# Optimization experiments

Hardware: AMD Instinct MI355X
Metric: run time of the kernel (lower is better)

The kernel has to match this reference:

```python
import jax, jax.numpy as jnp
import numpy as np

GH, GW = 16, 16          # group_size
DIM = 512
H = 8                    # num_heads
PD = DIM // 16           # pos_dim = (dim//4)//4 = 32
B = 256                  # number of groups (batch*windows)
N = GH * GW


def _make_bias_tables():
    # biases buffer: all 2D relative offsets, shape [(2GH-1)*(2GW-1), 2]
    h = np.arange(1 - GH, GH)
    w = np.arange(1 - GW, GW)
    bh, bw = np.meshgrid(h, w, indexing='ij')
    biases = np.stack([bh, bw]).reshape(2, -1).T.astype(np.float32)
    # relative_position_index: [N, N] lookup into the bias table
    ch, cw = np.meshgrid(np.arange(GH), np.arange(GW), indexing='ij')
    coords = np.stack([ch, cw]).reshape(2, -1)            # [2, N]
    rel = coords[:, :, None] - coords[:, None, :]         # [2, N, N]
    rel = rel.transpose(1, 2, 0).copy()                   # [N, N, 2]
    rel[:, :, 0] += GH - 1
    rel[:, :, 1] += GW - 1
    rel[:, :, 0] *= 2 * GW - 1
    idx = rel.sum(-1)
    return biases, idx.astype(np.int32)


def _ln(x, g, b, eps=1e-5):
    m = x.mean(-1, keepdims=True)
    v = ((x - m) ** 2).mean(-1, keepdims=True)
    return (x - m) / jnp.sqrt(v + eps) * g + b


def setup_inputs() -> dict:
    key = jax.random.key(0)
    ks = jax.random.split(key, 16)
    s = 0.02
    biases_np, idx_np = _make_bias_tables()
    return {
        'x': jax.random.normal(ks[0], (B, N, DIM), dtype=jnp.float32),
        'qkv_w': jax.random.normal(ks[1], (DIM, 3 * DIM), dtype=jnp.float32) * s,
        'qkv_b': jnp.zeros((3 * DIM,), jnp.float32),
        'proj_w': jax.random.normal(ks[2], (DIM, DIM), dtype=jnp.float32) * s,
        'proj_b': jnp.zeros((DIM,), jnp.float32),
        'p1_w': jax.random.normal(ks[3], (2, PD), dtype=jnp.float32) * s,
        'p1_b': jnp.zeros((PD,), jnp.float32),
        'g1': jnp.ones((PD,), jnp.float32), 'b1': jnp.zeros((PD,), jnp.float32),
        'p2_w': jax.random.normal(ks[4], (PD, PD), dtype=jnp.float32) * s,
        'p2_b': jnp.zeros((PD,), jnp.float32),
        'g2': jnp.ones((PD,), jnp.float32), 'b2': jnp.zeros((PD,), jnp.float32),
        'p3_w': jax.random.normal(ks[5], (PD, PD), dtype=jnp.float32) * s,
        'p3_b': jnp.zeros((PD,), jnp.float32),
        'g3': jnp.ones((PD,), jnp.float32), 'b3': jnp.zeros((PD,), jnp.float32),
        'p4_w': jax.random.normal(ks[6], (PD, H), dtype=jnp.float32) * s,
        'p4_b': jnp.zeros((H,), jnp.float32),
        'biases': jnp.asarray(biases_np),
        'rel_idx': jnp.asarray(idx_np),
    }


def reference(x, qkv_w, qkv_b, proj_w, proj_b,
              p1_w, p1_b, g1, b1, p2_w, p2_b, g2, b2,
              p3_w, p3_b, g3, b3, p4_w, p4_b, biases, rel_idx):
    Bn, Nn, C = x.shape
    hd = C // H
    scale = hd ** -0.5
    qkv = (x @ qkv_w + qkv_b).reshape(Bn, Nn, 3, H, hd).transpose(2, 0, 3, 1, 4)
    q, k, v = qkv[0] * scale, qkv[1], qkv[2]      # [B, H, N, hd]
    attn = jnp.einsum('bhnd,bhmd->bhnm', q, k)    # [B, H, N, N]
    # dynamic position bias MLP on the offset table
    h1 = jax.nn.relu(_ln(biases @ p1_w + p1_b, g1, b1))
    h2 = jax.nn.relu(_ln(h1 @ p2_w + p2_b, g2, b2))
    h3 = jax.nn.relu(_ln(h2 @ p3_w + p3_b, g3, b3))
    pos = h3 @ p4_w + p4_b                        # [L, H]
    rpb = pos[rel_idx.reshape(-1)].reshape(Nn, Nn, H).transpose(2, 0, 1)  # [H, N, N]
    attn = jax.nn.softmax(attn + rpb[None], axis=-1)
    out = jnp.einsum('bhnm,bhmd->bhnd', attn, v)
    out = out.transpose(0, 2, 1, 3).reshape(Bn, Nn, C)
    return out @ proj_w + proj_b
```

## Files before the change

kernel.cpp:

```cpp
#include <hip/hip_runtime.h>
#include <stdint.h>

typedef __bf16 bf16x8 __attribute__((ext_vector_type(8)));
typedef float  f32x4  __attribute__((ext_vector_type(4)));
typedef unsigned short ushort_t;

#define MFMA16(a,b,c) __builtin_amdgcn_mfma_f32_16x16x32_bf16((a),(b),(c),0,0,0)

#define GLOAD16(gsrc, ldst) \
    __builtin_amdgcn_global_load_lds((const __attribute__((address_space(1))) void*)(gsrc), \
                                     (__attribute__((address_space(3))) void*)(ldst), 16, 0, 0)

#define BATCH 256
#define NTOK  256
#define DIM   512
#define NH    8
#define HD    64
#define PD    32
#define LTAB  961

#define POS_OFF   0
#define RPB_OFF   32768
#define WQKV_OFF  (RPB_OFF + 2097152)
#define WPROJ_OFF (WQKV_OFF + 1572864)
#define QKV_OFF   (WPROJ_OFF + 524288)
#define AOUT_OFF  (QKV_OFF + 201326592)
#define XB_OFF    AOUT_OFF

__device__ __forceinline__ ushort_t f2bf(float f) {
    unsigned int u = __builtin_bit_cast(unsigned int, f);
    u += 0x7FFFu + ((u >> 16) & 1u);
    return (ushort_t)(u >> 16);
}

__global__ __launch_bounds__(256) void convert_x(
    const float* __restrict__ x, ushort_t* __restrict__ xb)
{
    size_t i = ((size_t)blockIdx.x * 256 + threadIdx.x) * 8;
    float4 f0 = *(const float4*)(x + i);
    float4 f1 = *(const float4*)(x + i + 4);
    uint4 o;
    o.x = (unsigned)f2bf(f0.x) | ((unsigned)f2bf(f0.y) << 16);
    o.y = (unsigned)f2bf(f0.z) | ((unsigned)f2bf(f0.w) << 16);
    o.z = (unsigned)f2bf(f1.x) | ((unsigned)f2bf(f1.y) << 16);
    o.w = (unsigned)f2bf(f1.z) | ((unsigned)f2bf(f1.w) << 16);
    *reinterpret_cast<uint4*>(xb + i) = o;
}

__global__ __launch_bounds__(256) void transpose_w(
    const float* __restrict__ src, ushort_t* __restrict__ dst, int K, int Nn)
{
    __shared__ ushort_t tile[64][65];
    int tiles_n = Nn >> 6;
    int tn = blockIdx.x % tiles_n, tk = blockIdx.x / tiles_n;
    int n0 = tn * 64, k0 = tk * 64;
    int t = threadIdx.x;
#pragma unroll
    for (int i = 0; i < 16; i++) {
        int idx = t + i * 256;
        int kl = idx >> 6, nl = idx & 63;
        tile[nl][kl] = f2bf(src[(size_t)(k0 + kl) * Nn + n0 + nl]);
    }
    __syncthreads();
#pragma unroll
    for (int i = 0; i < 16; i++) {
        int idx = t + i * 256;
        int nl = idx >> 6, kl = idx & 63;
        dst[(size_t)(n0 + nl) * K + k0 + kl] = tile[nl][kl];
    }
}

__device__ __forceinline__ float ln_relu_t(float h, int j,
                                           const float* __restrict__ g,
                                           const float* __restrict__ bb) {
    float m = h;
    m += __shfl_xor(m, 1); m += __shfl_xor(m, 2); m += __shfl_xor(m, 4);
    m += __shfl_xor(m, 8); m += __shfl_xor(m, 16);
    m *= (1.0f / PD);
    float d = h - m;
    float v = d * d;
    v += __shfl_xor(v, 1); v += __shfl_xor(v, 2); v += __shfl_xor(v, 4);
    v += __shfl_xor(v, 8); v += __shfl_xor(v, 16);
    v *= (1.0f / PD);
    float x = d * rsqrtf(v + 1e-5f) * g[j] + bb[j];
    return x > 0.f ? x : 0.f;
}

__global__ __launch_bounds__(256) void pos_mlp(
    const float* __restrict__ biases,
    const float* __restrict__ p1_w, const float* __restrict__ p1_b,
    const float* __restrict__ g1, const float* __restrict__ b1,
    const float* __restrict__ p2_w, const float* __restrict__ p2_b,
    const float* __restrict__ g2, const float* __restrict__ b2,
    const float* __restrict__ p3_w, const float* __restrict__ p3_b,
    const float* __restrict__ g3, const float* __restrict__ b3,
    const float* __restrict__ p4_w, const float* __restrict__ p4_b,
    float* __restrict__ pos)
{
    __shared__ float hs[8][33];
    int tid = threadIdx.x;
    int rl = tid >> 5, j = tid & 31;
    int r = blockIdx.x * 8 + rl;
    bool ok = r < LTAB;
    float c0 = ok ? biases[r * 2 + 0] : 0.f;
    float c1 = ok ? biases[r * 2 + 1] : 0.f;

    float h = c0 * p1_w[j] + c1 * p1_w[PD + j] + p1_b[j];
    h = ln_relu_t(h, j, g1, b1);

    hs[rl][j] = h;
    __syncthreads();
    float s = p2_b[j];
#pragma unroll
    for (int i = 0; i < PD; i++) s += hs[rl][i] * p2_w[i * PD + j];
    __syncthreads();
    h = ln_relu_t(s, j, g2, b2);

    hs[rl][j] = h;
    __syncthreads();
    s = p3_b[j];
#pragma unroll
    for (int i = 0; i < PD; i++) s += hs[rl][i] * p3_w[i * PD + j];
    __syncthreads();
    h = ln_relu_t(s, j, g3, b3);

    hs[rl][j] = h;
    __syncthreads();
    if (ok && j < NH) {
        float o = p4_b[j];
#pragma unroll
        for (int i = 0; i < PD; i++) o += hs[rl][i] * p4_w[i * NH + j];
        pos[r * NH + j] = o;
    }
}

__global__ __launch_bounds__(256) void rpb_gather(
    const float* __restrict__ pos, const int* __restrict__ rel_idx,
    float* __restrict__ rpb)
{
    int i = blockIdx.x * 256 + threadIdx.x;
    int idx = rel_idx[i];
#pragma unroll
    for (int hh = 0; hh < NH; hh++) rpb[(size_t)hh * 65536 + i] = pos[idx * NH + hh];
}

__global__ __launch_bounds__(512, 1) void qkv_gemm(
    const ushort_t* __restrict__ xb, const ushort_t* __restrict__ wT,
    const float* __restrict__ qkv_b, ushort_t* __restrict__ qkvb)
{
    __shared__ ushort_t As[2][256 * 64];
    __shared__ ushort_t Bs[2][256 * 64];
    int t = threadIdx.x;
    int bid = blockIdx.x;
    int wgid = (bid & 7) * 192 + (bid >> 3);
    int mt = wgid / 6, nt = wgid % 6;
    int m0 = mt * 256, n0 = nt * 256;
    int lane = t & 63, w = t >> 6;
    int wm = w >> 2, wn = w & 3;
    int lr = lane & 15, lk = lane >> 4;
    int srow8 = lane >> 3;
    int sch = ((lane & 7) ^ srow8) * 8;
    const ushort_t* Asrc = xb + (size_t)(m0 + srow8) * 512 + sch;
    const ushort_t* Bsrc = wT + (size_t)(n0 + srow8) * 512 + sch;
    int arw = w & 3;
    int ch0 = ((lk) ^ (lr & 7)) * 8;
    int ch1 = ((4 + lk) ^ (lr & 7)) * 8;
    int arow = wm * 128 + lr;
    int brow = wn * 64 + lr;

    f32x4 acc[8][4];
#pragma unroll
    for (int fr = 0; fr < 8; fr++)
#pragma unroll
        for (int fc = 0; fc < 4; fc++) acc[fr][fc] = (f32x4){0.f, 0.f, 0.f, 0.f};

#define QSTAGE(buf, kt) do { \
    if (w < 4) { \
        _Pragma("unroll") \
        for (int i_ = 0; i_ < 8; i_++) { \
            int rb_ = arw * 64 + i_ * 8; \
            GLOAD16(Asrc + (size_t)rb_ * 512 + (kt) * 64, &As[buf][rb_ * 64]); \
        } \
    } else { \
        _Pragma("unroll") \
        for (int i_ = 0; i_ < 8; i_++) { \
            int rb_ = arw * 64 + i_ * 8; \
            GLOAD16(Bsrc + (size_t)rb_ * 512 + (kt) * 64, &Bs[buf][rb_ * 64]); \
        } \
    } } while (0)

    QSTAGE(0, 0);
    asm volatile("s_waitcnt vmcnt(0)" ::: "memory");
    __syncthreads();
    for (int kt = 0; kt < 8; ++kt) {
        int cb = kt & 1;
        if (kt < 7) QSTAGE(cb ^ 1, kt + 1);
#pragma unroll
        for (int kh = 0; kh < 2; kh++) {
            int ch = kh ? ch1 : ch0;
            bf16x8 a[8], b[4];
#pragma unroll
            for (int fr = 0; fr < 8; fr++)
                a[fr] = *reinterpret_cast<const bf16x8*>(&As[cb][(arow + fr * 16) * 64 + ch]);
#pragma unroll
            for (int fc = 0; fc < 4; fc++)
                b[fc] = *reinterpret_cast<const bf16x8*>(&Bs[cb][(brow + fc * 16) * 64 + ch]);
#pragma unroll
            for (int fr = 0; fr < 8; fr++)
#pragma unroll
                for (int fc = 0; fc < 4; fc++)
                    acc[fr][fc] = MFMA16(a[fr], b[fc], acc[fr][fc]);
        }
        if (kt < 7) {
            asm volatile("s_waitcnt vmcnt(0)" ::: "memory");
            __syncthreads();
        }
    }
#undef QSTAGE

    int s = n0 >> 9;
    int bg = m0 >> 8;
    if (s < 2) {
        float sc = (s == 0) ? 0.125f : 1.0f;
#pragma unroll
        for (int fc = 0; fc < 4; fc++) {
            int n = n0 + wn * 64 + fc * 16 + lr;
            float bias = qkv_b[n];
            int hh = (n >> 6) & 7, d = n & 63;
            ushort_t* dst = qkvb + ((((size_t)s * 256 + bg) * 8 + hh) * 256) * 64 + d;
#pragma unroll
            for (int fr = 0; fr < 8; fr++)
#pragma unroll
                for (int r = 0; r < 4; r++) {
                    int tok = wm * 128 + fr * 16 + lk * 4 + r;
                    dst[(size_t)tok * 64] = f2bf((acc[fr][fc][r] + bias) * sc);
                }
        }
    } else {
#pragma unroll
        for (int fc = 0; fc < 4; fc++) {
            int n = n0 + wn * 64 + fc * 16 + lr;
            float bias = qkv_b[n];
            int hh = (n >> 6) & 7, d = n & 63;
            ushort_t* dst = qkvb + ((((size_t)512 + bg) * 8 + hh) * 64 + d) * 256;
#pragma unroll
            for (int fr = 0; fr < 8; fr++) {
                int tok = wm * 128 + fr * 16 + lk * 4;
                uint2 pk;
                pk.x = (unsigned)f2bf(acc[fr][fc][0] + bias) |
                       ((unsigned)f2bf(acc[fr][fc][1] + bias) << 16);
                pk.y = (unsigned)f2bf(acc[fr][fc][2] + bias) |
                       ((unsigned)f2bf(acc[fr][fc][3] + bias) << 16);
                *reinterpret_cast<uint2*>(dst + tok) = pk;
            }
        }
    }
}

__global__ __launch_bounds__(256) void attn_kernel(
    const ushort_t* __restrict__ qkvb, const float* __restrict__ rpb,
    ushort_t* __restrict__ aout)
{
    __shared__ ushort_t Ps[4][32][40];
    __shared__ ushort_t Os[4][16 * 72];
    int t = threadIdx.x, lane = t & 63, w = t >> 6;
    int bid = blockIdx.x;
    int qh = bid & 1; int bh = bid >> 1; int hh = bh & 7; int bg = bh >> 3;
    const ushort_t* Qg  = qkvb + (((size_t)bg * 8 + hh) * 256) * 64;
    const ushort_t* Kg  = qkvb + (((size_t)(256 + bg) * 8 + hh) * 256) * 64;
    const ushort_t* VTg = qkvb + (((size_t)(512 + bg) * 8 + hh) * 64) * 256;
    int lr = lane & 15, lk = lane >> 4;
    int qrow0 = qh * 128 + w * 32;

    bf16x8 qf[2][2];
#pragma unroll
    for (int fr = 0; fr < 2; fr++)
#pragma unroll
        for (int kc = 0; kc < 2; kc++)
            qf[fr][kc] = *reinterpret_cast<const bf16x8*>(
                Qg + (size_t)(qrow0 + fr * 16 + lr) * 64 + kc * 32 + lk * 8);

    f32x4 oacc[2][4];
    float rsum[2][4];
#pragma unroll
    for (int fr = 0; fr < 2; fr++) {
#pragma unroll
        for (int fc = 0; fc < 4; fc++) oacc[fr][fc] = (f32x4){0.f, 0.f, 0.f, 0.f};
#pragma unroll
        for (int r = 0; r < 4; r++) rsum[fr][r] = 0.f;
    }

    for (int kt = 0; kt < 8; ++kt) {
        f32x4 sacc[2][2];
#pragma unroll
        for (int fr = 0; fr < 2; fr++)
#pragma unroll
            for (int fc = 0; fc < 2; fc++) sacc[fr][fc] = (f32x4){0.f, 0.f, 0.f, 0.f};
#pragma unroll
        for (int kc = 0; kc < 2; kc++) {
            bf16x8 kb0 = *reinterpret_cast<const bf16x8*>(
                Kg + (size_t)(kt * 32 + lr) * 64 + kc * 32 + lk * 8);
            bf16x8 kb1 = *reinterpret_cast<const bf16x8*>(
                Kg + (size_t)(kt * 32 + 16 + lr) * 64 + kc * 32 + lk * 8);
            sacc[0][0] = MFMA16(qf[0][kc], kb0, sacc[0][0]);
            sacc[0][1] = MFMA16(qf[0][kc], kb1, sacc[0][1]);
            sacc[1][0] = MFMA16(qf[1][kc], kb0, sacc[1][0]);
            sacc[1][1] = MFMA16(qf[1][kc], kb1, sacc[1][1]);
        }
#pragma unroll
        for (int fr = 0; fr < 2; fr++)
#pragma unroll
            for (int fc = 0; fc < 2; fc++)
#pragma unroll
                for (int r = 0; r < 4; r++) {
                    int row = qrow0 + fr * 16 + lk * 4 + r;
                    int col = kt * 32 + fc * 16 + lr;
                    float lg = sacc[fr][fc][r] + rpb[((size_t)hh * 256 + row) * 256 + col];
                    float p = __expf(lg);
                    rsum[fr][r] += p;
                    Ps[w][fr * 16 + lk * 4 + r][fc * 16 + lr] = f2bf(p);
                }
        bf16x8 pa[2], vb[4];
#pragma unroll
        for (int fr = 0; fr < 2; fr++)
            pa[fr] = *reinterpret_cast<const bf16x8*>(&Ps[w][fr * 16 + lr][lk * 8]);
#pragma unroll
        for (int fc = 0; fc < 4; fc++)
            vb[fc] = *reinterpret_cast<const bf16x8*>(
                VTg + (size_t)(fc * 16 + lr) * 256 + kt * 32 + lk * 8);
#pragma unroll
        for (int fr = 0; fr < 2; fr++)
#pragma unroll
            for (int fc = 0; fc < 4; fc++)
                oacc[fr][fc] = MFMA16(pa[fr], vb[fc], oacc[fr][fc]);
    }
    float rinv[2][4];
#pragma unroll
    for (int fr = 0; fr < 2; fr++)
#pragma unroll
        for (int r = 0; r < 4; r++) {
            float s = rsum[fr][r];
            s += __shfl_xor(s, 1); s += __shfl_xor(s, 2);
            s += __shfl_xor(s, 4); s += __shfl_xor(s, 8);
            rinv[fr][r] = __frcp_rn(s);
        }
#pragma unroll
    for (int fr = 0; fr < 2; fr++) {
#pragma unroll
        for (int fc = 0; fc < 4; fc++)
#pragma unroll
            for (int r = 0; r < 4; r++)
                Os[w][(lk * 4 + r) * 72 + fc * 16 + lr] = f2bf(oacc[fr][fc][r] * rinv[fr][r]);
#pragma unroll
        for (int ii = 0; ii < 2; ii++) {
            int j = lane + ii * 64;
            int row = j >> 3, ch = j & 7;
            uint4 v = *reinterpret_cast<const uint4*>(&Os[w][row * 72 + ch * 8]);
            *reinterpret_cast<uint4*>(
                aout + ((size_t)(bg * 256 + qrow0 + fr * 16 + row)) * 512 + hh * 64 + ch * 8) = v;
        }
    }
}

__global__ __launch_bounds__(512, 1) void proj_gemm(
    const ushort_t* __restrict__ ain, const ushort_t* __restrict__ wT,
    const float* __restrict__ proj_b, float* __restrict__ out)
{
    __shared__ ushort_t As[2][256 * 64];
    __shared__ ushort_t Bs[2][256 * 64];
    int t = threadIdx.x;
    int bid = blockIdx.x;
    int wgid = (bid & 7) * 64 + (bid >> 3);
    int mt = wgid / 2, nt = wgid % 2;
    int m0 = mt * 256, n0 = nt * 256;
    int lane = t & 63, w = t >> 6;
    int wm = w >> 2, wn = w & 3;
    int lr = lane & 15, lk = lane >> 4;
    int srow8 = lane >> 3;
    int sch = ((lane & 7) ^ srow8) * 8;
    const ushort_t* Asrc = ain + (size_t)(m0 + srow8) * 512 + sch;
    const ushort_t* Bsrc = wT + (size_t)(n0 + srow8) * 512 + sch;
    int arw = w & 3;
    int ch0 = ((lk) ^ (lr & 7)) * 8;
    int ch1 = ((4 + lk) ^ (lr & 7)) * 8;
    int arow = wm * 128 + lr;
    int brow = wn * 64 + lr;

    f32x4 acc[8][4];
#pragma unroll
    for (int fr = 0; fr < 8; fr++)
#pragma unroll
        for (int fc = 0; fc < 4; fc++) acc[fr][fc] = (f32x4){0.f, 0.f, 0.f, 0.f};

#define PSTAGE(buf, kt) do { \
    if (w < 4) { \
        _Pragma("unroll") \
        for (int i_ = 0; i_ < 8; i_++) { \
            int rb_ = arw * 64 + i_ * 8; \
            GLOAD16(Asrc + (size_t)rb_ * 512 + (kt) * 64, &As[buf][rb_ * 64]); \
        } \
    } else { \
        _Pragma("unroll") \
        for (int i_ = 0; i_ < 8; i_++) { \
            int rb_ = arw * 64 + i_ * 8; \
            GLOAD16(Bsrc + (size_t)rb_ * 512 + (kt) * 64, &Bs[buf][rb_ * 64]); \
        } \
    } } while (0)

    PSTAGE(0, 0);
    asm volatile("s_waitcnt vmcnt(0)" ::: "memory");
    __syncthreads();
    for (int kt = 0; kt < 8; ++kt) {
        int cb = kt & 1;
        if (kt < 7) PSTAGE(cb ^ 1, kt + 1);
#pragma unroll
        for (int kh = 0; kh < 2; kh++) {
            int ch = kh ? ch1 : ch0;
            bf16x8 a[8], b[4];
#pragma unroll
            for (int fr = 0; fr < 8; fr++)
                a[fr] = *reinterpret_cast<const bf16x8*>(&As[cb][(arow + fr * 16) * 64 + ch]);
#pragma unroll
            for (int fc = 0; fc < 4; fc++)
                b[fc] = *reinterpret_cast<const bf16x8*>(&Bs[cb][(brow + fc * 16) * 64 + ch]);
#pragma unroll
            for (int fr = 0; fr < 8; fr++)
#pragma unroll
                for (int fc = 0; fc < 4; fc++)
                    acc[fr][fc] = MFMA16(a[fr], b[fc], acc[fr][fc]);
        }
        if (kt < 7) {
            asm volatile("s_waitcnt vmcnt(0)" ::: "memory");
            __syncthreads();
        }
    }
#undef PSTAGE
#pragma unroll
    for (int fc = 0; fc < 4; fc++) {
        int n = n0 + wn * 64 + fc * 16 + lr;
        float bias = proj_b[n];
#pragma unroll
        for (int fr = 0; fr < 8; fr++)
#pragma unroll
            for (int r = 0; r < 4; r++) {
                int m = m0 + wm * 128 + fr * 16 + lk * 4 + r;
                out[(size_t)m * 512 + n] = acc[fr][fc][r] + bias;
            }
    }
}

extern "C" void kernel_launch(void* const* d_in, const int* in_sizes, int n_in,
                              void* d_out, int out_size, void* d_ws, size_t ws_size,
                              hipStream_t stream) {
    const float* x      = (const float*)d_in[0];
    const float* qkv_w  = (const float*)d_in[1];
    const float* qkv_b  = (const float*)d_in[2];
    const float* proj_w = (const float*)d_in[3];
    const float* proj_b = (const float*)d_in[4];
    const float* p1_w = (const float*)d_in[5];
    const float* p1_b = (const float*)d_in[6];
    const float* g1   = (const float*)d_in[7];
    const float* b1   = (const float*)d_in[8];
    const float* p2_w = (const float*)d_in[9];
    const float* p2_b = (const float*)d_in[10];
    const float* g2   = (const float*)d_in[11];
    const float* b2   = (const float*)d_in[12];
    const float* p3_w = (const float*)d_in[13];
    const float* p3_b = (const float*)d_in[14];
    const float* g3   = (const float*)d_in[15];
    const float* b3   = (const float*)d_in[16];
    const float* p4_w = (const float*)d_in[17];
    const float* p4_b = (const float*)d_in[18];
    const float* biases  = (const float*)d_in[19];
    const int*   rel_idx = (const int*)d_in[20];
    float* out = (float*)d_out;

    char* ws = (char*)d_ws;
    float*    pos    = (float*)(ws + POS_OFF);
    float*    rpb    = (float*)(ws + RPB_OFF);
    ushort_t* wqkvT  = (ushort_t*)(ws + WQKV_OFF);
    ushort_t* wprojT = (ushort_t*)(ws + WPROJ_OFF);
    ushort_t* qkvb   = (ushort_t*)(ws + QKV_OFF);
    ushort_t* aoutb  = (ushort_t*)(ws + AOUT_OFF);
    ushort_t* xb     = (ushort_t*)(ws + XB_OFF);

    convert_x<<<dim3(16384), dim3(256), 0, stream>>>(x, xb);
    transpose_w<<<dim3(24 * 8), dim3(256), 0, stream>>>(qkv_w, wqkvT, 512, 1536);
    transpose_w<<<dim3(8 * 8), dim3(256), 0, stream>>>(proj_w, wprojT, 512, 512);
    pos_mlp<<<dim3(121), dim3(256), 0, stream>>>(biases, p1_w, p1_b, g1, b1,
                                                 p2_w, p2_b, g2, b2,
                                                 p3_w, p3_b, g3, b3,
                                                 p4_w, p4_b, pos);
    rpb_gather<<<dim3(256), dim3(256), 0, stream>>>(pos, rel_idx, rpb);
    qkv_gemm<<<dim3(1536), dim3(512), 0, stream>>>(xb, wqkvT, qkv_b, qkvb);
    attn_kernel<<<dim3(4096), dim3(256), 0, stream>>>(qkvb, rpb, aoutb);
    proj_gemm<<<dim3(512), dim3(512), 0, stream>>>(aoutb, wprojT, proj_b, out);
}
```

Before: 383.0 us.

## Deepen qkv/proj GEMM pipeline with half-K LDS stages and MFMA priority

The qkv and proj GEMMs now split each 64-wide K tile into two 32-wide half stages. All waves issue loads for both A and B, and loads run up to three half-stages ahead, with partial vmcnt waits in place of the full drain. The LDS swizzle changes to fit 32-element rows, and s_setprio raises wave priority around the MFMA blocks. The goal is to hide global-to-LDS latency behind compute, at the cost of more barriers and tighter waitcnt bookkeeping, where a miscount could cause races.

```diff
diff --git a/kernel.cpp b/kernel.cpp
--- a/kernel.cpp
+++ b/kernel.cpp
@@ -148,8 +148,8 @@
     const ushort_t* __restrict__ xb, const ushort_t* __restrict__ wT,
     const float* __restrict__ qkv_b, ushort_t* __restrict__ qkvb)
 {
-    __shared__ ushort_t As[2][256 * 64];
-    __shared__ ushort_t Bs[2][256 * 64];
+    __shared__ ushort_t As[2][2][8192];
+    __shared__ ushort_t Bs[2][2][8192];
     int t = threadIdx.x;
     int bid = blockIdx.x;
     int wgid = (bid & 7) * 192 + (bid >> 3);
@@ -158,13 +158,11 @@
     int lane = t & 63, w = t >> 6;
     int wm = w >> 2, wn = w & 3;
     int lr = lane & 15, lk = lane >> 4;
-    int srow8 = lane >> 3;
-    int sch = ((lane & 7) ^ srow8) * 8;
-    const ushort_t* Asrc = xb + (size_t)(m0 + srow8) * 512 + sch;
-    const ushort_t* Bsrc = wT + (size_t)(n0 + srow8) * 512 + sch;
-    int arw = w & 3;
-    int ch0 = ((lk) ^ (lr & 7)) * 8;
-    int ch1 = ((4 + lk) ^ (lr & 7)) * 8;
+    int srow = lane >> 2;
+    int sch = ((lane & 3) ^ ((lane >> 3) & 3)) * 8;
+    const ushort_t* Asrc = xb + (size_t)(m0 + srow) * 512 + sch;
+    const ushort_t* Bsrc = wT + (size_t)(n0 + srow) * 512 + sch;
+    int rch = (lk ^ ((lr >> 1) & 3)) * 8;
     int arow = wm * 128 + lr;
     int brow = wn * 64 + lr;
 
@@ -174,49 +172,53 @@
 #pragma unroll
         for (int fc = 0; fc < 4; fc++) acc[fr][fc] = (f32x4){0.f, 0.f, 0.f, 0.f};
 
-#define QSTAGE(buf, kt) do { \
-    if (w < 4) { \
+#define QSTAGE(buf, kt, kh) do { \
+    _Pragma("unroll") \
+    for (int j_ = 0; j_ < 2; j_++) { \
+        int r0_ = (w * 2 + j_) * 16; \
+        GLOAD16(Asrc + (size_t)r0_ * 512 + (kt) * 64 + (kh) * 32, &As[buf][kh][r0_ * 32]); \
+        GLOAD16(Bsrc + (size_t)r0_ * 512 + (kt) * 64 + (kh) * 32, &Bs[buf][kh][r0_ * 32]); \
+    } } while (0)
+
+#define QCOMP(cb, kh) do { \
+    bf16x8 a_[8], b_[4]; \
+    _Pragma("unroll") \
+    for (int fr = 0; fr < 8; fr++) \
+        a_[fr] = *reinterpret_cast<const bf16x8*>(&As[cb][kh][(arow + fr * 16) * 32 + rch]); \
+    _Pragma("unroll") \
+    for (int fc = 0; fc < 4; fc++) \
+        b_[fc] = *reinterpret_cast<const bf16x8*>(&Bs[cb][kh][(brow + fc * 16) * 32 + rch]); \
+    __builtin_amdgcn_s_setprio(1); \
+    _Pragma("unroll") \
+    for (int fr = 0; fr < 8; fr++) \
         _Pragma("unroll") \
-        for (int i_ = 0; i_ < 8; i_++) { \
-            int rb_ = arw * 64 + i_ * 8; \
-            GLOAD16(Asrc + (size_t)rb_ * 512 + (kt) * 64, &As[buf][rb_ * 64]); \
-        } \
-    } else { \
-        _Pragma("unroll") \
-        for (int i_ = 0; i_ < 8; i_++) { \
-            int rb_ = arw * 64 + i_ * 8; \
-            GLOAD16(Bsrc + (size_t)rb_ * 512 + (kt) * 64, &Bs[buf][rb_ * 64]); \
-        } \
-    } } while (0)
-
-    QSTAGE(0, 0);
-    asm volatile("s_waitcnt vmcnt(0)" ::: "memory");
+        for (int fc = 0; fc < 4; fc++) \
+            acc[fr][fc] = MFMA16(a_[fr], b_[fc], acc[fr][fc]); \
+    __builtin_amdgcn_s_setprio(0); \
+    } while (0)
+
+    QSTAGE(0, 0, 0);
+    QSTAGE(0, 0, 1);
+    QSTAGE(1, 1, 0);
+    asm volatile("s_waitcnt vmcnt(8)" ::: "memory");
     __syncthreads();
     for (int kt = 0; kt < 8; ++kt) {
         int cb = kt & 1;
-        if (kt < 7) QSTAGE(cb ^ 1, kt + 1);
-#pragma unroll
-        for (int kh = 0; kh < 2; kh++) {
-            int ch = kh ? ch1 : ch0;
-            bf16x8 a[8], b[4];
-#pragma unroll
-            for (int fr = 0; fr < 8; fr++)
-                a[fr] = *reinterpret_cast<const bf16x8*>(&As[cb][(arow + fr * 16) * 64 + ch]);
-#pragma unroll
-            for (int fc = 0; fc < 4; fc++)
-                b[fc] = *reinterpret_cast<const bf16x8*>(&Bs[cb][(brow + fc * 16) * 64 + ch]);
-#pragma unroll
-            for (int fr = 0; fr < 8; fr++)
-#pragma unroll
-                for (int fc = 0; fc < 4; fc++)
-                    acc[fr][fc] = MFMA16(a[fr], b[fc], acc[fr][fc]);
-        }
+        if (kt + 1 < 8) QSTAGE((kt + 1) & 1, kt + 1, 1);
+        QCOMP(cb, 0);
+        if (kt < 7) asm volatile("s_waitcnt vmcnt(8)" ::: "memory");
+        else        asm volatile("s_waitcnt vmcnt(0)" ::: "memory");
+        __syncthreads();
+        if (kt + 2 < 8) QSTAGE(cb, kt + 2, 0);
+        QCOMP(cb, 1);
         if (kt < 7) {
-            asm volatile("s_waitcnt vmcnt(0)" ::: "memory");
+            if (kt == 6) asm volatile("s_waitcnt vmcnt(4)" ::: "memory");
+            else         asm volatile("s_waitcnt vmcnt(8)" ::: "memory");
             __syncthreads();
         }
     }
 #undef QSTAGE
+#undef QCOMP
 
     int s = n0 >> 9;
     int bg = m0 >> 8;
@@ -366,8 +368,8 @@
     const ushort_t* __restrict__ ain, const ushort_t* __restrict__ wT,
     const float* __restrict__ proj_b, float* __restrict__ out)
 {
-    __shared__ ushort_t As[2][256 * 64];
-    __shared__ ushort_t Bs[2][256 * 64];
+    __shared__ ushort_t As[2][2][8192];
+    __shared__ ushort_t Bs[2][2][8192];
     int t = threadIdx.x;
     int bid = blockIdx.x;
     int wgid = (bid & 7) * 64 + (bid >> 3);
@@ -376,13 +378,11 @@
     int lane = t & 63, w = t >> 6;
     int wm = w >> 2, wn = w & 3;
     int lr = lane & 15, lk = lane >> 4;
-    int srow8 = lane >> 3;
-    int sch = ((lane & 7) ^ srow8) * 8;
-    const ushort_t* Asrc = ain + (size_t)(m0 + srow8) * 512 + sch;
-    const ushort_t* Bsrc = wT + (size_t)(n0 + srow8) * 512 + sch;
-    int arw = w & 3;
-    int ch0 = ((lk) ^ (lr & 7)) * 8;
-    int ch1 = ((4 + lk) ^ (lr & 7)) * 8;
+    int srow = lane >> 2;
+    int sch = ((lane & 3) ^ ((lane >> 3) & 3)) * 8;
+    const ushort_t* Asrc = ain + (size_t)(m0 + srow) * 512 + sch;
+    const ushort_t* Bsrc = wT + (size_t)(n0 + srow) * 512 + sch;
+    int rch = (lk ^ ((lr >> 1) & 3)) * 8;
     int arow = wm * 128 + lr;
     int brow = wn * 64 + lr;
 
@@ -392,49 +392,54 @@
 #pragma unroll
         for (int fc = 0; fc < 4; fc++) acc[fr][fc] = (f32x4){0.f, 0.f, 0.f, 0.f};
 
-#define PSTAGE(buf, kt) do { \
-    if (w < 4) { \
+#define PSTAGE(buf, kt, kh) do { \
+    _Pragma("unroll") \
+    for (int j_ = 0; j_ < 2; j_++) { \
+        int r0_ = (w * 2 + j_) * 16; \
+        GLOAD16(Asrc + (size_t)r0_ * 512 + (kt) * 64 + (kh) * 32, &As[buf][kh][r0_ * 32]); \
+        GLOAD16(Bsrc + (size_t)r0_ * 512 + (kt) * 64 + (kh) * 32, &Bs[buf][kh][r0_ * 32]); \
+    } } while (0)
+
+#define PCOMP(cb, kh) do { \
+    bf16x8 a_[8], b_[4]; \
+    _Pragma("unroll") \
+    for (int fr = 0; fr < 8; fr++) \
+        a_[fr] = *reinterpret_cast<const bf16x8*>(&As[cb][kh][(arow + fr * 16) * 32 + rch]); \
+    _Pragma("unroll") \
+    for (int fc = 0; fc < 4; fc++) \
+        b_[fc] = *reinterpret_cast<const bf16x8*>(&Bs[cb][kh][(brow + fc * 16) * 32 + rch]); \
+    __builtin_amdgcn_s_setprio(1); \
+    _Pragma("unroll") \
+    for (int fr = 0; fr < 8; fr++) \
         _Pragma("unroll") \
-        for (int i_ = 0; i_ < 8; i_++) { \
-            int rb_ = arw * 64 + i_ * 8; \
-            GLOAD16(Asrc + (size_t)rb_ * 512 + (kt) * 64, &As[buf][rb_ * 64]); \
-        } \
-    } else { \
-        _Pragma("unroll") \
-        for (int i_ = 0; i_ < 8; i_++) { \
-            int rb_ = arw * 64 + i_ * 8; \
-            GLOAD16(Bsrc + (size_t)rb_ * 512 + (kt) * 64, &Bs[buf][rb_ * 64]); \
-        } \
-    } } while (0)
-
-    PSTAGE(0, 0);
-    asm volatile("s_waitcnt vmcnt(0)" ::: "memory");
+        for (int fc = 0; fc < 4; fc++) \
+            acc[fr][fc] = MFMA16(a_[fr], b_[fc], acc[fr][fc]); \
+    __builtin_amdgcn_s_setprio(0); \
+    } while (0)
+
+    PSTAGE(0, 0, 0);
+    PSTAGE(0, 0, 1);
+    PSTAGE(1, 1, 0);
+    asm volatile("s_waitcnt vmcnt(8)" ::: "memory");
     __syncthreads();
     for (int kt = 0; kt < 8; ++kt) {
         int cb = kt & 1;
-        if (kt < 7) PSTAGE(cb ^ 1, kt + 1);
-#pragma unroll
-        for (int kh = 0; kh < 2; kh++) {
-            int ch = kh ? ch1 : ch0;
-            bf16x8 a[8], b[4];
-#pragma unroll
-            for (int fr = 0; fr < 8; fr++)
-                a[fr] = *reinterpret_cast<const bf16x8*>(&As[cb][(arow + fr * 16) * 64 + ch]);
-#pragma unroll
-            for (int fc = 0; fc < 4; fc++)
-                b[fc] = *reinterpret_cast<const bf16x8*>(&Bs[cb][(brow + fc * 16) * 64 + ch]);
-#pragma unroll
-            for (int fr = 0; fr < 8; fr++)
-#pragma unroll
-                for (int fc = 0; fc < 4; fc++)
-                    acc[fr][fc] = MFMA16(a[fr], b[fc], acc[fr][fc]);
-        }
+        if (kt + 1 < 8) PSTAGE((kt + 1) & 1, kt + 1, 1);
+        PCOMP(cb, 0);
+        if (kt < 7) asm volatile("s_waitcnt vmcnt(8)" ::: "memory");
+        else        asm volatile("s_waitcnt vmcnt(0)" ::: "memory");
+        __syncthreads();
+        if (kt + 2 < 8) PSTAGE(cb, kt + 2, 0);
+        PCOMP(cb, 1);
         if (kt < 7) {
-            asm volatile("s_waitcnt vmcnt(0)" ::: "memory");
+            if (kt == 6) asm volatile("s_waitcnt vmcnt(4)" ::: "memory");
+            else         asm volatile("s_waitcnt vmcnt(8)" ::: "memory");
             __syncthreads();
         }
     }
 #undef PSTAGE
+#undef PCOMP
+
 #pragma unroll
     for (int fc = 0; fc < 4; fc++) {
         int n = n0 + wn * 64 + fc * 16 + lr;
```

Result: slower. 419.4 us (+9.5%).
